# Kernel optimization log

Measured on AMD Instinct MI355X. Metric: run time of the kernel, lower is better.

## Reference

```python
import jax, jax.numpy as jnp
import numpy as np

EPS = 1e-3  # batch_norm_epsilon


def _lstm_last(xs, W, U, b):
    """Keras-order LSTM (gates i,f,g,o); returns last hidden state [B,H]."""
    B = xs.shape[0]
    H = U.shape[0]

    def step(carry, xt):
        h, c = carry
        z = xt @ W + h @ U + b  # [B, 4H]
        i, f, g, o = jnp.split(z, 4, axis=-1)
        i = jax.nn.sigmoid(i)
        f = jax.nn.sigmoid(f)
        g = jnp.tanh(g)
        o = jax.nn.sigmoid(o)
        c = f * c + i * g
        h = o * jnp.tanh(c)
        return (h, c), None

    init = (jnp.zeros((B, H), xs.dtype), jnp.zeros((B, H), xs.dtype))
    (h, _), _ = jax.lax.scan(step, init, jnp.swapaxes(xs, 0, 1))
    return h


def setup_inputs() -> dict:
    key = jax.random.key(0)
    ks = jax.random.split(key, 10)
    B, T, C, H = 32, 512, 512, 512
    s_in = 1.0 / np.sqrt(C)
    s_rec = 1.0 / np.sqrt(H)
    return {
        "x": jax.random.normal(ks[0], (B, T, C), jnp.float32),
        # BatchNorm params (inference / moving stats)
        "gamma": jnp.ones((C,), jnp.float32),
        "beta": jnp.zeros((C,), jnp.float32),
        "moving_mean": jax.random.normal(ks[1], (C,), jnp.float32) * 0.1,
        "moving_var": jnp.abs(jax.random.normal(ks[2], (C,), jnp.float32)) * 0.1 + 1.0,
        # forward-direction LSTM
        "Wf": jax.random.normal(ks[3], (C, 4 * H), jnp.float32) * s_in,
        "Uf": jax.random.normal(ks[4], (H, 4 * H), jnp.float32) * s_rec,
        "bf": jnp.zeros((4 * H,), jnp.float32),
        # backward-direction LSTM
        "Wb": jax.random.normal(ks[5], (C, 4 * H), jnp.float32) * s_in,
        "Ub": jax.random.normal(ks[6], (H, 4 * H), jnp.float32) * s_rec,
        "bb": jnp.zeros((4 * H,), jnp.float32),
    }


def reference(x, gamma, beta, moving_mean, moving_var, Wf, Uf, bf, Wb, Ub, bb):
    # BatchNorm (inference) over last axis
    inv = jax.lax.rsqrt(moving_var + EPS)
    xn = (x - moving_mean) * inv * gamma + beta
    # Bidirectional LSTM, merge_mode='concat', return_sequences=False
    h_fwd = _lstm_last(xn, Wf, Uf, bf)
    h_bwd = _lstm_last(xn[:, ::-1, :], Wb, Ub, bb)
    return jnp.concatenate([h_fwd, h_bwd], axis=-1)  # [B, 2H]
```

## Files before the change

### kernel.cpp

```cpp
#include <hip/hip_runtime.h>
#include <stdint.h>

typedef __attribute__((ext_vector_type(8))) short short8;
typedef __attribute__((ext_vector_type(4))) float f32x4;
typedef __attribute__((ext_vector_type(2))) float f32x2;

#define NB 32
#define NT 512
#define NC 512
#define NH 512
#define NG 2048
#define WPD 32
#define NWG 64
#define UPW 16

__device__ __forceinline__ float bf2f(unsigned short u){
  union { unsigned int i; float f; } v; v.i = ((unsigned int)u) << 16; return v.f;
}
__device__ __forceinline__ unsigned short f2bf(float f){
  union { float f; unsigned int i; } v; v.f = f;
  unsigned int r = v.i + 0x7fffu + ((v.i >> 16) & 1u);
  return (unsigned short)(r >> 16);
}
__device__ __forceinline__ bool dt_fp32(const void* gamma){
  return ((const unsigned short*)gamma)[0] != 0x3F80;
}
__device__ __forceinline__ float ldv(const void* p, size_t i, bool f32){
  return f32 ? ((const float*)p)[i] : bf2f(((const unsigned short*)p)[i]);
}
__device__ __forceinline__ short8 frag_from_f32(const float* p){
  short8 r;
  #pragma unroll
  for (int j = 0; j < 8; ++j) r[j] = (short)f2bf(p[j]);
  return r;
}
__device__ __forceinline__ float sigm(float x){ return 1.f/(1.f + __expf(-x)); }
__device__ __forceinline__ float tanh_(float x){ return 1.f - 2.f/(1.f + __expf(2.f*x)); }

__device__ __forceinline__ unsigned int llc_load_u32(const unsigned int* p){
  unsigned int r;
  asm volatile("global_load_dword %0, %1, off sc0 sc1\n\ts_waitcnt vmcnt(0)"
               : "=v"(r) : "v"(p) : "memory");
  return r;
}
__device__ __forceinline__ void llc_store_u32(unsigned int* p, unsigned int v){
  asm volatile("global_store_dword %0, %1, off sc0 sc1" :: "v"(p), "v"(v) : "memory");
}
__device__ __forceinline__ void llc_load_hfrags(const unsigned short* p0,
                                                const unsigned short* p1,
                                                short8 hf[4][2]){
  asm volatile(
    "global_load_dwordx4 %0, %8, off sc0 sc1\n\t"
    "global_load_dwordx4 %1, %8, off offset:64 sc0 sc1\n\t"
    "global_load_dwordx4 %2, %8, off offset:128 sc0 sc1\n\t"
    "global_load_dwordx4 %3, %8, off offset:192 sc0 sc1\n\t"
    "global_load_dwordx4 %4, %9, off sc0 sc1\n\t"
    "global_load_dwordx4 %5, %9, off offset:64 sc0 sc1\n\t"
    "global_load_dwordx4 %6, %9, off offset:128 sc0 sc1\n\t"
    "global_load_dwordx4 %7, %9, off offset:192 sc0 sc1\n\t"
    "s_waitcnt vmcnt(0)"
    : "=&v"(hf[0][0]), "=&v"(hf[1][0]), "=&v"(hf[2][0]), "=&v"(hf[3][0]),
      "=&v"(hf[0][1]), "=&v"(hf[1][1]), "=&v"(hf[2][1]), "=&v"(hf[3][1])
    : "v"(p0), "v"(p1) : "memory");
}

__global__ void k_init(const void* __restrict__ gamma,
                       const void* __restrict__ beta,
                       const void* __restrict__ mmean,
                       const void* __restrict__ mvar,
                       float* __restrict__ scale, float* __restrict__ shift,
                       unsigned short* __restrict__ hbuf, unsigned int* __restrict__ flags){
  bool f32 = dt_fp32(gamma);
  int tid = blockIdx.x * 256 + threadIdx.x;
  if (blockIdx.x == 0){
    for (int c = threadIdx.x; c < NC; c += 256){
      float s = ldv(gamma, c, f32) * rsqrtf(ldv(mvar, c, f32) + 1e-3f);
      scale[c] = s;
      shift[c] = ldv(beta, c, f32) - ldv(mmean, c, f32) * s;
    }
    if (threadIdx.x < 64) flags[threadIdx.x] = 0u;
  }
  for (int i = tid; i < 2*2*NB*NH; i += gridDim.x * 256) hbuf[i] = 0;
}

__global__ void k_xcast(const void* __restrict__ x, const void* __restrict__ gamma,
                        unsigned short* __restrict__ x2){
  bool f32 = dt_fp32(gamma);
  int i = blockIdx.x * 256 + threadIdx.x;
  int c8 = i & 63;
  int rest = i >> 6;
  int t = rest & (NT - 1);
  int b = rest >> 9;
  size_t src = ((size_t)b * NT + t) * NC + c8 * 8;
  size_t dst = ((size_t)t * NB + b) * NC + c8 * 8;
  unsigned int pk[4];
  if (f32){
    const float* p = (const float*)x + src;
    #pragma unroll
    for (int j = 0; j < 4; ++j)
      pk[j] = (unsigned int)f2bf(p[2*j]) | ((unsigned int)f2bf(p[2*j+1]) << 16);
  } else {
    __builtin_memcpy(pk, (const unsigned short*)x + src, 16);
  }
  __builtin_memcpy(x2 + dst, pk, 16);
}

__global__ void k_bias(const void* __restrict__ Wf, const void* __restrict__ Wb,
                       const void* __restrict__ bfv, const void* __restrict__ bbv,
                       const void* __restrict__ gamma,
                       const float* __restrict__ shift, float* __restrict__ bias){
  bool f32 = dt_fp32(gamma);
  int id = blockIdx.x * 256 + threadIdx.x;
  int dir = id >> 11, n = id & 2047;
  const void* W = dir ? Wb : Wf;
  const void* b = dir ? bbv : bfv;
  float acc = ldv(b, n, f32);
  for (int c = 0; c < NC; ++c) acc += shift[c] * ldv(W, (size_t)c * NG + n, f32);
  bias[id] = acc;
}

__global__ __launch_bounds__(256, 1) void k_lstm(
    const void* __restrict__ x, const unsigned short* __restrict__ x2, int use_x2,
    const void* __restrict__ Wf, const void* __restrict__ Uf,
    const void* __restrict__ Wb, const void* __restrict__ Ub,
    const void* __restrict__ gamma,
    const float* __restrict__ scale, const float* __restrict__ bias,
    unsigned short* __restrict__ hbuf, unsigned int* __restrict__ flags,
    void* __restrict__ out){
  __shared__ float zbuf[4][NB][68];

  bool f32 = dt_fp32(gamma);
  int wg   = blockIdx.x;
  int dir  = wg & 1;
  int wgd  = wg >> 1;
  int ubase = wgd * UPW;
  const void* W = dir ? Wb : Wf;
  const void* U = dir ? Ub : Uf;
  int tid  = threadIdx.x;
  int lane = tid & 63, wave = tid >> 6;
  int m = lane & 15, q = lane >> 4;

  short8 bw[4][4], bu[4][4];
  #pragma unroll
  for (int kcl = 0; kcl < 4; ++kcl){
    int kc = wave * 4 + kcl;
    #pragma unroll
    for (int g = 0; g < 4; ++g){
      int col = g * NH + ubase + m;
      short8 vw, vu;
      #pragma unroll
      for (int j = 0; j < 8; ++j){
        int k = kc * 32 + q * 8 + j;
        vu[j] = (short)f2bf(ldv(U, (size_t)k * NG + col, f32));
        vw[j] = (short)f2bf(scale[k] * ldv(W, (size_t)k * NG + col, f32));
      }
      bw[kcl][g] = vw; bu[kcl][g] = vu;
    }
  }

  int pb = tid >> 3, pu2 = (tid & 7) * 2;
  float bias_r[2][4];
  #pragma unroll
  for (int g = 0; g < 4; ++g){
    bias_r[0][g] = bias[dir * NG + g * NH + ubase + pu2];
    bias_r[1][g] = bias[dir * NG + g * NH + ubase + pu2 + 1];
  }
  float cst[2] = {0.f, 0.f};

  unsigned int* myflags = flags + dir * 32;
  unsigned int* ownflag = myflags + wgd;
  unsigned short* hb0 = hbuf + (size_t)dir * 2 * NB * NH;

  short8 xf[4][2];
  {
    int tt0 = dir ? (NT - 1) : 0;
    #pragma unroll
    for (int kcl = 0; kcl < 4; ++kcl){
      int kc = wave * 4 + kcl;
      #pragma unroll
      for (int mt = 0; mt < 2; ++mt){
        if (use_x2){
          size_t xi = ((size_t)tt0 * NB + (mt * 16 + m)) * NC + kc * 32 + q * 8;
          __builtin_memcpy(&xf[kcl][mt], x2 + xi, 16);
        } else {
          size_t xi = ((size_t)(mt * 16 + m) * NT + tt0) * NC + kc * 32 + q * 8;
          if (f32) xf[kcl][mt] = frag_from_f32((const float*)x + xi);
          else     __builtin_memcpy(&xf[kcl][mt], (const unsigned short*)x + xi, 16);
        }
      }
    }
  }

  #pragma unroll 1
  for (int t = 0; t < NT; ++t){
    const unsigned short* hcur = hb0 + (size_t)(t & 1) * NB * NH;
    unsigned short* hnext = hb0 + (size_t)((t + 1) & 1) * NB * NH;

    f32x4 acc[4][2];
    #pragma unroll
    for (int g = 0; g < 4; ++g){
      acc[g][0] = (f32x4){0.f,0.f,0.f,0.f};
      acc[g][1] = (f32x4){0.f,0.f,0.f,0.f};
    }

    #pragma unroll
    for (int kcl = 0; kcl < 4; ++kcl)
      #pragma unroll
      for (int mt = 0; mt < 2; ++mt)
        #pragma unroll
        for (int g = 0; g < 4; ++g)
          acc[g][mt] = __builtin_amdgcn_mfma_f32_16x16x32_bf16(xf[kcl][mt], bw[kcl][g], acc[g][mt], 0, 0, 0);

    if (t < NT - 1){
      int ttn = dir ? (NT - 2 - t) : (t + 1);
      #pragma unroll
      for (int kcl = 0; kcl < 4; ++kcl){
        int kc = wave * 4 + kcl;
        #pragma unroll
        for (int mt = 0; mt < 2; ++mt){
          if (use_x2){
            size_t xi = ((size_t)ttn * NB + (mt * 16 + m)) * NC + kc * 32 + q * 8;
            __builtin_memcpy(&xf[kcl][mt], x2 + xi, 16);
          } else {
            size_t xi = ((size_t)(mt * 16 + m) * NT + ttn) * NC + kc * 32 + q * 8;
            if (f32) xf[kcl][mt] = frag_from_f32((const float*)x + xi);
            else     __builtin_memcpy(&xf[kcl][mt], (const unsigned short*)x + xi, 16);
          }
        }
      }
    }

    if (t > 0){
      unsigned int tgt = (unsigned int)t;
      while (true){
        unsigned int v = llc_load_u32(myflags + (lane & 31));
        if (__all((int)(v >= tgt))) break;
      }
    }

    short8 hf[4][2];
    llc_load_hfrags(hcur + (size_t)m * NH + wave * 128 + q * 8,
                    hcur + (size_t)(16 + m) * NH + wave * 128 + q * 8, hf);
    #pragma unroll
    for (int kcl = 0; kcl < 4; ++kcl)
      #pragma unroll
      for (int mt = 0; mt < 2; ++mt)
        #pragma unroll
        for (int g = 0; g < 4; ++g)
          acc[g][mt] = __builtin_amdgcn_mfma_f32_16x16x32_bf16(hf[kcl][mt], bu[kcl][g], acc[g][mt], 0, 0, 0);

    #pragma unroll
    for (int g = 0; g < 4; ++g)
      #pragma unroll
      for (int mt = 0; mt < 2; ++mt)
        #pragma unroll
        for (int r = 0; r < 4; ++r)
          zbuf[wave][mt * 16 + q * 4 + r][g * 16 + m] = acc[g][mt][r];
    __syncthreads();

    float z[2][4];
    #pragma unroll
    for (int g = 0; g < 4; ++g){ z[0][g] = bias_r[0][g]; z[1][g] = bias_r[1][g]; }
    #pragma unroll
    for (int w = 0; w < 4; ++w)
      #pragma unroll
      for (int g = 0; g < 4; ++g){
        f32x2 v = *(const f32x2*)&zbuf[w][pb][g * 16 + pu2];
        z[0][g] += v[0]; z[1][g] += v[1];
      }
    float hv[2];
    #pragma unroll
    for (int j = 0; j < 2; ++j){
      float iv = sigm(z[j][0]), fv = sigm(z[j][1]), gv = tanh_(z[j][2]), ov = sigm(z[j][3]);
      cst[j] = fv * cst[j] + iv * gv;
      hv[j] = ov * tanh_(cst[j]);
    }

    if (t == NT - 1){
      size_t o0 = (size_t)pb * (2 * NH) + dir * NH + ubase + pu2;
      if (f32){
        f32x2 ov2 = {hv[0], hv[1]};
        *(f32x2*)&((float*)out)[o0] = ov2;
      } else {
        unsigned int pk = (unsigned int)f2bf(hv[0]) | ((unsigned int)f2bf(hv[1]) << 16);
        *(unsigned int*)&((unsigned short*)out)[o0] = pk;
      }
      break;
    }

    {
      unsigned int pk = (unsigned int)f2bf(hv[0]) | ((unsigned int)f2bf(hv[1]) << 16);
      llc_store_u32((unsigned int*)(hnext + (size_t)pb * NH + ubase + pu2), pk);
    }

    __syncthreads();
    if (tid == 0) llc_store_u32(ownflag, (unsigned int)(t + 1));
  }
}

extern "C" void kernel_launch(void* const* d_in, const int* in_sizes, int n_in,
                              void* d_out, int out_size, void* d_ws, size_t ws_size,
                              hipStream_t stream){
  const void* x     = d_in[0];
  const void* gamma = d_in[1];
  const void* beta  = d_in[2];
  const void* mmean = d_in[3];
  const void* mvar  = d_in[4];
  const void* Wf    = d_in[5];
  const void* Uf    = d_in[6];
  const void* bfv   = d_in[7];
  const void* Wb    = d_in[8];
  const void* Ub    = d_in[9];
  const void* bbv   = d_in[10];

  char* ws = (char*)d_ws;
  float* scale = (float*)(ws + 0);
  float* shift = (float*)(ws + 2048);
  float* bias  = (float*)(ws + 4096);
  unsigned short* hbuf = (unsigned short*)(ws + 20480);
  unsigned int* flags  = (unsigned int*)(ws + 20480 + 131072);
  size_t x2_off = 20480 + 131072 + 4096;
  unsigned short* x2 = (unsigned short*)(ws + x2_off);
  size_t x2_bytes = (size_t)NT * NB * NC * 2;
  int use_x2 = (ws_size >= x2_off + x2_bytes) ? 1 : 0;

  hipLaunchKernelGGL(k_init, dim3(64),  dim3(256), 0, stream,
                     gamma, beta, mmean, mvar, scale, shift, hbuf, flags);
  if (use_x2)
    hipLaunchKernelGGL(k_xcast, dim3((NB*NT*NC/8)/256), dim3(256), 0, stream,
                       x, gamma, x2);
  hipLaunchKernelGGL(k_bias, dim3(16),  dim3(256), 0, stream,
                     Wf, Wb, bfv, bbv, gamma, shift, bias);
  hipLaunchKernelGGL(k_lstm, dim3(NWG), dim3(256), 0, stream,
                     x, x2, use_x2, Wf, Uf, Wb, Ub, gamma, scale, bias, hbuf, flags, d_out);
}
```

Before: 2.052 ms.

## Replace per-step flag barrier with step-tagged hidden-state words polled directly

Each hidden value is now stored as a 32-bit word holding bf16 data in the high half and the timestep tag in the low half. Consumers poll the hidden-state fragments themselves until every tag matches, instead of spinning on per-workgroup flags and then loading h. This removes the separate flag store, the extra __syncthreads before it, and a dependent load round trip. The hidden loads are also issued before the input-projection MFMAs so they overlap that work, and zbuf is double-buffered by step parity so the trailing barrier can go. The cost is twice the hidden-buffer traffic, more registers for the raw words, and repeated reissue of 16 loads while the tags are not yet current.

```diff
diff --git a/kernel.cpp b/kernel.cpp
--- a/kernel.cpp
+++ b/kernel.cpp
@@ -4,6 +4,8 @@
 typedef __attribute__((ext_vector_type(8))) short short8;
 typedef __attribute__((ext_vector_type(4))) float f32x4;
 typedef __attribute__((ext_vector_type(2))) float f32x2;
+typedef __attribute__((ext_vector_type(4))) unsigned int u32x4;
+typedef __attribute__((ext_vector_type(2))) unsigned int u32x2;
 
 #define NB 32
 #define NT 512
@@ -37,31 +39,46 @@
 __device__ __forceinline__ float sigm(float x){ return 1.f/(1.f + __expf(-x)); }
 __device__ __forceinline__ float tanh_(float x){ return 1.f - 2.f/(1.f + __expf(2.f*x)); }
 
-__device__ __forceinline__ unsigned int llc_load_u32(const unsigned int* p){
-  unsigned int r;
-  asm volatile("global_load_dword %0, %1, off sc0 sc1\n\ts_waitcnt vmcnt(0)"
-               : "=v"(r) : "v"(p) : "memory");
-  return r;
-}
-__device__ __forceinline__ void llc_store_u32(unsigned int* p, unsigned int v){
-  asm volatile("global_store_dword %0, %1, off sc0 sc1" :: "v"(p), "v"(v) : "memory");
-}
-__device__ __forceinline__ void llc_load_hfrags(const unsigned short* p0,
-                                                const unsigned short* p1,
-                                                short8 hf[4][2]){
+__device__ __forceinline__ unsigned int permhi(unsigned int hi, unsigned int lo){
+  return __builtin_amdgcn_perm(hi, lo, 0x07060302u);
+}
+
+__device__ __forceinline__ void poll_issue(const unsigned int* p0, const unsigned int* p1,
+                                           u32x4 r[16]){
   asm volatile(
-    "global_load_dwordx4 %0, %8, off sc0 sc1\n\t"
-    "global_load_dwordx4 %1, %8, off offset:64 sc0 sc1\n\t"
-    "global_load_dwordx4 %2, %8, off offset:128 sc0 sc1\n\t"
-    "global_load_dwordx4 %3, %8, off offset:192 sc0 sc1\n\t"
-    "global_load_dwordx4 %4, %9, off sc0 sc1\n\t"
-    "global_load_dwordx4 %5, %9, off offset:64 sc0 sc1\n\t"
-    "global_load_dwordx4 %6, %9, off offset:128 sc0 sc1\n\t"
-    "global_load_dwordx4 %7, %9, off offset:192 sc0 sc1\n\t"
-    "s_waitcnt vmcnt(0)"
-    : "=&v"(hf[0][0]), "=&v"(hf[1][0]), "=&v"(hf[2][0]), "=&v"(hf[3][0]),
-      "=&v"(hf[0][1]), "=&v"(hf[1][1]), "=&v"(hf[2][1]), "=&v"(hf[3][1])
+    "global_load_dwordx4 %0, %16, off sc0 sc1\n\t"
+    "global_load_dwordx4 %1, %16, off offset:16 sc0 sc1\n\t"
+    "global_load_dwordx4 %2, %16, off offset:128 sc0 sc1\n\t"
+    "global_load_dwordx4 %3, %16, off offset:144 sc0 sc1\n\t"
+    "global_load_dwordx4 %4, %16, off offset:256 sc0 sc1\n\t"
+    "global_load_dwordx4 %5, %16, off offset:272 sc0 sc1\n\t"
+    "global_load_dwordx4 %6, %16, off offset:384 sc0 sc1\n\t"
+    "global_load_dwordx4 %7, %16, off offset:400 sc0 sc1\n\t"
+    "global_load_dwordx4 %8, %17, off sc0 sc1\n\t"
+    "global_load_dwordx4 %9, %17, off offset:16 sc0 sc1\n\t"
+    "global_load_dwordx4 %10, %17, off offset:128 sc0 sc1\n\t"
+    "global_load_dwordx4 %11, %17, off offset:144 sc0 sc1\n\t"
+    "global_load_dwordx4 %12, %17, off offset:256 sc0 sc1\n\t"
+    "global_load_dwordx4 %13, %17, off offset:272 sc0 sc1\n\t"
+    "global_load_dwordx4 %14, %17, off offset:384 sc0 sc1\n\t"
+    "global_load_dwordx4 %15, %17, off offset:400 sc0 sc1"
+    : "=&v"(r[0]), "=&v"(r[1]), "=&v"(r[2]), "=&v"(r[3]),
+      "=&v"(r[4]), "=&v"(r[5]), "=&v"(r[6]), "=&v"(r[7]),
+      "=&v"(r[8]), "=&v"(r[9]), "=&v"(r[10]), "=&v"(r[11]),
+      "=&v"(r[12]), "=&v"(r[13]), "=&v"(r[14]), "=&v"(r[15])
     : "v"(p0), "v"(p1) : "memory");
+}
+__device__ __forceinline__ void poll_wait(u32x4 r[16]){
+  asm volatile("s_waitcnt vmcnt(0)"
+    : "+v"(r[0]), "+v"(r[1]), "+v"(r[2]), "+v"(r[3]),
+      "+v"(r[4]), "+v"(r[5]), "+v"(r[6]), "+v"(r[7]),
+      "+v"(r[8]), "+v"(r[9]), "+v"(r[10]), "+v"(r[11]),
+      "+v"(r[12]), "+v"(r[13]), "+v"(r[14]), "+v"(r[15])
+    :: "memory");
+}
+__device__ __forceinline__ void llc_store_b64(unsigned int* p, unsigned int lo, unsigned int hi){
+  u32x2 v; v[0] = lo; v[1] = hi;
+  asm volatile("global_store_dwordx2 %0, %1, off sc0 sc1" :: "v"(p), "v"(v) : "memory");
 }
 
 __global__ void k_init(const void* __restrict__ gamma,
@@ -69,7 +86,7 @@
                        const void* __restrict__ mmean,
                        const void* __restrict__ mvar,
                        float* __restrict__ scale, float* __restrict__ shift,
-                       unsigned short* __restrict__ hbuf, unsigned int* __restrict__ flags){
+                       unsigned int* __restrict__ hbuf){
   bool f32 = dt_fp32(gamma);
   int tid = blockIdx.x * 256 + threadIdx.x;
   if (blockIdx.x == 0){
@@ -78,9 +95,8 @@
       scale[c] = s;
       shift[c] = ldv(beta, c, f32) - ldv(mmean, c, f32) * s;
     }
-    if (threadIdx.x < 64) flags[threadIdx.x] = 0u;
-  }
-  for (int i = tid; i < 2*2*NB*NH; i += gridDim.x * 256) hbuf[i] = 0;
+  }
+  for (int i = tid; i < 2*2*NB*NH; i += gridDim.x * 256) hbuf[i] = 0u;
 }
 
 __global__ void k_xcast(const void* __restrict__ x, const void* __restrict__ gamma,
@@ -125,9 +141,8 @@
     const void* __restrict__ Wb, const void* __restrict__ Ub,
     const void* __restrict__ gamma,
     const float* __restrict__ scale, const float* __restrict__ bias,
-    unsigned short* __restrict__ hbuf, unsigned int* __restrict__ flags,
-    void* __restrict__ out){
-  __shared__ float zbuf[4][NB][68];
+    unsigned int* __restrict__ hbuf, void* __restrict__ out){
+  __shared__ float zbuf[2][4][NB][68];
 
   bool f32 = dt_fp32(gamma);
   int wg   = blockIdx.x;
@@ -167,9 +182,7 @@
   }
   float cst[2] = {0.f, 0.f};
 
-  unsigned int* myflags = flags + dir * 32;
-  unsigned int* ownflag = myflags + wgd;
-  unsigned short* hb0 = hbuf + (size_t)dir * 2 * NB * NH;
+  unsigned int* hb32 = hbuf + (size_t)dir * 2 * NB * NH;
 
   short8 xf[4][2];
   {
@@ -193,8 +206,13 @@
 
   #pragma unroll 1
   for (int t = 0; t < NT; ++t){
-    const unsigned short* hcur = hb0 + (size_t)(t & 1) * NB * NH;
-    unsigned short* hnext = hb0 + (size_t)((t + 1) & 1) * NB * NH;
+    const unsigned int* hcur = hb32 + (size_t)(t & 1) * NB * NH;
+    unsigned int* hnext = hb32 + (size_t)((t + 1) & 1) * NB * NH;
+
+    u32x4 raw[16];
+    const unsigned int* p0 = hcur + (size_t)m * NH + wave * 128 + q * 8;
+    const unsigned int* p1 = p0 + (size_t)16 * NH;
+    poll_issue(p0, p1, raw);
 
     f32x4 acc[4][2];
     #pragma unroll
@@ -229,33 +247,46 @@
         }
       }
     }
-
-    if (t > 0){
-      unsigned int tgt = (unsigned int)t;
+    __builtin_amdgcn_sched_barrier(0);
+
+    {
+      unsigned int tg = (unsigned int)t;
       while (true){
-        unsigned int v = llc_load_u32(myflags + (lane & 31));
-        if (__all((int)(v >= tgt))) break;
-      }
-    }
-
-    short8 hf[4][2];
-    llc_load_hfrags(hcur + (size_t)m * NH + wave * 128 + q * 8,
-                    hcur + (size_t)(16 + m) * NH + wave * 128 + q * 8, hf);
-    #pragma unroll
-    for (int kcl = 0; kcl < 4; ++kcl)
+        poll_wait(raw);
+        unsigned int d = 0;
+        #pragma unroll
+        for (int i = 0; i < 16; ++i)
+          d |= (raw[i][0] ^ tg) | (raw[i][1] ^ tg) | (raw[i][2] ^ tg) | (raw[i][3] ^ tg);
+        if (__all((int)((d & 0xffffu) == 0u))) break;
+        poll_issue(p0, p1, raw);
+      }
+    }
+
+    #pragma unroll
+    for (int kcl = 0; kcl < 4; ++kcl){
+      #pragma unroll
+      for (int mt = 0; mt < 2; ++mt){
+        union { short8 s; unsigned int w[4]; } u;
+        u32x4 a = raw[mt * 8 + kcl * 2];
+        u32x4 b = raw[mt * 8 + kcl * 2 + 1];
+        u.w[0] = permhi(a[1], a[0]);
+        u.w[1] = permhi(a[3], a[2]);
+        u.w[2] = permhi(b[1], b[0]);
+        u.w[3] = permhi(b[3], b[2]);
+        #pragma unroll
+        for (int g = 0; g < 4; ++g)
+          acc[g][mt] = __builtin_amdgcn_mfma_f32_16x16x32_bf16(u.s, bu[kcl][g], acc[g][mt], 0, 0, 0);
+      }
+    }
+
+    int par = t & 1;
+    #pragma unroll
+    for (int g = 0; g < 4; ++g)
       #pragma unroll
       for (int mt = 0; mt < 2; ++mt)
         #pragma unroll
-        for (int g = 0; g < 4; ++g)
-          acc[g][mt] = __builtin_amdgcn_mfma_f32_16x16x32_bf16(hf[kcl][mt], bu[kcl][g], acc[g][mt], 0, 0, 0);
-
-    #pragma unroll
-    for (int g = 0; g < 4; ++g)
-      #pragma unroll
-      for (int mt = 0; mt < 2; ++mt)
-        #pragma unroll
         for (int r = 0; r < 4; ++r)
-          zbuf[wave][mt * 16 + q * 4 + r][g * 16 + m] = acc[g][mt][r];
+          zbuf[par][wave][mt * 16 + q * 4 + r][g * 16 + m] = acc[g][mt][r];
     __syncthreads();
 
     float z[2][4];
@@ -265,7 +296,7 @@
     for (int w = 0; w < 4; ++w)
       #pragma unroll
       for (int g = 0; g < 4; ++g){
-        f32x2 v = *(const f32x2*)&zbuf[w][pb][g * 16 + pu2];
+        f32x2 v = *(const f32x2*)&zbuf[par][w][pb][g * 16 + pu2];
         z[0][g] += v[0]; z[1][g] += v[1];
       }
     float hv[2];
@@ -289,12 +320,11 @@
     }
 
     {
-      unsigned int pk = (unsigned int)f2bf(hv[0]) | ((unsigned int)f2bf(hv[1]) << 16);
-      llc_store_u32((unsigned int*)(hnext + (size_t)pb * NH + ubase + pu2), pk);
-    }
-
-    __syncthreads();
-    if (tid == 0) llc_store_u32(ownflag, (unsigned int)(t + 1));
+      unsigned int tag1 = (unsigned int)(t + 1);
+      unsigned int w0 = ((unsigned int)f2bf(hv[0]) << 16) | tag1;
+      unsigned int w1 = ((unsigned int)f2bf(hv[1]) << 16) | tag1;
+      llc_store_b64(hnext + (size_t)pb * NH + ubase + pu2, w0, w1);
+    }
   }
 }
 
@@ -317,20 +347,19 @@
   float* scale = (float*)(ws + 0);
   float* shift = (float*)(ws + 2048);
   float* bias  = (float*)(ws + 4096);
-  unsigned short* hbuf = (unsigned short*)(ws + 20480);
-  unsigned int* flags  = (unsigned int*)(ws + 20480 + 131072);
-  size_t x2_off = 20480 + 131072 + 4096;
+  unsigned int* hbuf = (unsigned int*)(ws + 20480);
+  size_t x2_off = 20480 + 262144;
   unsigned short* x2 = (unsigned short*)(ws + x2_off);
   size_t x2_bytes = (size_t)NT * NB * NC * 2;
   int use_x2 = (ws_size >= x2_off + x2_bytes) ? 1 : 0;
 
   hipLaunchKernelGGL(k_init, dim3(64),  dim3(256), 0, stream,
-                     gamma, beta, mmean, mvar, scale, shift, hbuf, flags);
+                     gamma, beta, mmean, mvar, scale, shift, hbuf);
   if (use_x2)
     hipLaunchKernelGGL(k_xcast, dim3((NB*NT*NC/8)/256), dim3(256), 0, stream,
                        x, gamma, x2);
   hipLaunchKernelGGL(k_bias, dim3(16),  dim3(256), 0, stream,
                      Wf, Wb, bfv, bbv, gamma, shift, bias);
   hipLaunchKernelGGL(k_lstm, dim3(NWG), dim3(256), 0, stream,
-                     x, x2, use_x2, Wf, Uf, Wb, Ub, gamma, scale, bias, hbuf, flags, d_out);
-}
+                     x, x2, use_x2, Wf, Uf, Wb, Ub, gamma, scale, bias, hbuf, d_out);
+}
```

After: 2.812 ms. 37.0% more time.

## Fuse bias into LSTM kernel and switch to per-wave flags with pipelined polling

Applied to the files above, without the earlier changes.

Drops the separate bias-reduction kernel. The shift·W bias term is now accumulated during the weight-fragment load in the LSTM kernel and reduced with shuffles and shared memory. The block-wide barrier before the step flag is replaced by per-wave flags: each wave publishes its own completion and polls only the flags of the waves whose h slice it consumes. Flag polling keeps two loads in flight, and zbuf is double-buffered by step parity so the trailing barrier can go. This targets per-step synchronisation latency in the serial recurrence, at the cost of more flag traffic and subtler memory-ordering reasoning.

```diff
diff --git a/kernel.cpp b/kernel.cpp
--- a/kernel.cpp
+++ b/kernel.cpp
@@ -37,12 +37,6 @@
 __device__ __forceinline__ float sigm(float x){ return 1.f/(1.f + __expf(-x)); }
 __device__ __forceinline__ float tanh_(float x){ return 1.f - 2.f/(1.f + __expf(2.f*x)); }
 
-__device__ __forceinline__ unsigned int llc_load_u32(const unsigned int* p){
-  unsigned int r;
-  asm volatile("global_load_dword %0, %1, off sc0 sc1\n\ts_waitcnt vmcnt(0)"
-               : "=v"(r) : "v"(p) : "memory");
-  return r;
-}
 __device__ __forceinline__ void llc_store_u32(unsigned int* p, unsigned int v){
   asm volatile("global_store_dword %0, %1, off sc0 sc1" :: "v"(p), "v"(v) : "memory");
 }
@@ -78,7 +72,7 @@
       scale[c] = s;
       shift[c] = ldv(beta, c, f32) - ldv(mmean, c, f32) * s;
     }
-    if (threadIdx.x < 64) flags[threadIdx.x] = 0u;
+    flags[threadIdx.x] = 0u;
   }
   for (int i = tid; i < 2*2*NB*NH; i += gridDim.x * 256) hbuf[i] = 0;
 }
@@ -105,29 +99,16 @@
   __builtin_memcpy(x2 + dst, pk, 16);
 }
 
-__global__ void k_bias(const void* __restrict__ Wf, const void* __restrict__ Wb,
-                       const void* __restrict__ bfv, const void* __restrict__ bbv,
-                       const void* __restrict__ gamma,
-                       const float* __restrict__ shift, float* __restrict__ bias){
-  bool f32 = dt_fp32(gamma);
-  int id = blockIdx.x * 256 + threadIdx.x;
-  int dir = id >> 11, n = id & 2047;
-  const void* W = dir ? Wb : Wf;
-  const void* b = dir ? bbv : bfv;
-  float acc = ldv(b, n, f32);
-  for (int c = 0; c < NC; ++c) acc += shift[c] * ldv(W, (size_t)c * NG + n, f32);
-  bias[id] = acc;
-}
-
 __global__ __launch_bounds__(256, 1) void k_lstm(
     const void* __restrict__ x, const unsigned short* __restrict__ x2, int use_x2,
     const void* __restrict__ Wf, const void* __restrict__ Uf,
     const void* __restrict__ Wb, const void* __restrict__ Ub,
+    const void* __restrict__ bfv, const void* __restrict__ bbv,
     const void* __restrict__ gamma,
-    const float* __restrict__ scale, const float* __restrict__ bias,
+    const float* __restrict__ scale, const float* __restrict__ shift,
     unsigned short* __restrict__ hbuf, unsigned int* __restrict__ flags,
     void* __restrict__ out){
-  __shared__ float zbuf[4][NB][68];
+  __shared__ float zbuf[2][4][NB][68];
 
   bool f32 = dt_fp32(gamma);
   int wg   = blockIdx.x;
@@ -136,11 +117,13 @@
   int ubase = wgd * UPW;
   const void* W = dir ? Wb : Wf;
   const void* U = dir ? Ub : Uf;
+  const void* bvec = dir ? bbv : bfv;
   int tid  = threadIdx.x;
   int lane = tid & 63, wave = tid >> 6;
   int m = lane & 15, q = lane >> 4;
 
   short8 bw[4][4], bu[4][4];
+  float bp[4] = {0.f, 0.f, 0.f, 0.f};
   #pragma unroll
   for (int kcl = 0; kcl < 4; ++kcl){
     int kc = wave * 4 + kcl;
@@ -151,24 +134,44 @@
       #pragma unroll
       for (int j = 0; j < 8; ++j){
         int k = kc * 32 + q * 8 + j;
+        float wraw = ldv(W, (size_t)k * NG + col, f32);
         vu[j] = (short)f2bf(ldv(U, (size_t)k * NG + col, f32));
-        vw[j] = (short)f2bf(scale[k] * ldv(W, (size_t)k * NG + col, f32));
+        vw[j] = (short)f2bf(scale[k] * wraw);
+        bp[g] += shift[k] * wraw;
       }
       bw[kcl][g] = vw; bu[kcl][g] = vu;
     }
   }
+
+  #pragma unroll
+  for (int g = 0; g < 4; ++g){
+    bp[g] += __shfl_xor(bp[g], 16);
+    bp[g] += __shfl_xor(bp[g], 32);
+  }
+  float* bred = &zbuf[0][0][0][0];
+  if (q == 0){
+    #pragma unroll
+    for (int g = 0; g < 4; ++g) bred[wave * 64 + g * 16 + m] = bp[g];
+  }
+  __syncthreads();
 
   int pb = tid >> 3, pu2 = (tid & 7) * 2;
   float bias_r[2][4];
   #pragma unroll
-  for (int g = 0; g < 4; ++g){
-    bias_r[0][g] = bias[dir * NG + g * NH + ubase + pu2];
-    bias_r[1][g] = bias[dir * NG + g * NH + ubase + pu2 + 1];
-  }
+  for (int j = 0; j < 2; ++j)
+    #pragma unroll
+    for (int g = 0; g < 4; ++g){
+      float acc = ldv(bvec, g * NH + ubase + pu2 + j, f32);
+      #pragma unroll
+      for (int w = 0; w < 4; ++w) acc += bred[w * 64 + g * 16 + pu2 + j];
+      bias_r[j][g] = acc;
+    }
+  __syncthreads();
   float cst[2] = {0.f, 0.f};
 
-  unsigned int* myflags = flags + dir * 32;
-  unsigned int* ownflag = myflags + wgd;
+  unsigned int* myflags = flags + dir * 128;
+  unsigned int* ownflag = myflags + wgd * 4 + wave;
+  const unsigned int* fp = myflags + wave * 32 + (lane & 31);
   unsigned short* hb0 = hbuf + (size_t)dir * 2 * NB * NH;
 
   short8 xf[4][2];
@@ -190,6 +193,8 @@
       }
     }
   }
+
+  unsigned int fl0 = 0xffffffffu, fl1 = 0xffffffffu;
 
   #pragma unroll 1
   for (int t = 0; t < NT; ++t){
@@ -229,18 +234,26 @@
         }
       }
     }
+    __builtin_amdgcn_sched_barrier(0);
 
     if (t > 0){
       unsigned int tgt = (unsigned int)t;
+      asm volatile("global_load_dword %0, %1, off sc0 sc1" : "=v"(fl0) : "v"(fp) : "memory");
+      asm volatile("global_load_dword %0, %1, off sc0 sc1" : "=v"(fl1) : "v"(fp) : "memory");
       while (true){
-        unsigned int v = llc_load_u32(myflags + (lane & 31));
-        if (__all((int)(v >= tgt))) break;
+        asm volatile("s_waitcnt vmcnt(1)" : "+v"(fl0) :: "memory");
+        if (__all((int)(fl0 >= tgt))) break;
+        asm volatile("global_load_dword %0, %1, off sc0 sc1" : "=v"(fl0) : "v"(fp) : "memory");
+        asm volatile("s_waitcnt vmcnt(1)" : "+v"(fl1) :: "memory");
+        if (__all((int)(fl1 >= tgt))) break;
+        asm volatile("global_load_dword %0, %1, off sc0 sc1" : "=v"(fl1) : "v"(fp) : "memory");
       }
     }
 
     short8 hf[4][2];
     llc_load_hfrags(hcur + (size_t)m * NH + wave * 128 + q * 8,
                     hcur + (size_t)(16 + m) * NH + wave * 128 + q * 8, hf);
+    asm volatile("" : "+v"(fl0), "+v"(fl1));
     #pragma unroll
     for (int kcl = 0; kcl < 4; ++kcl)
       #pragma unroll
@@ -249,13 +262,14 @@
         for (int g = 0; g < 4; ++g)
           acc[g][mt] = __builtin_amdgcn_mfma_f32_16x16x32_bf16(hf[kcl][mt], bu[kcl][g], acc[g][mt], 0, 0, 0);
 
+    int par = t & 1;
     #pragma unroll
     for (int g = 0; g < 4; ++g)
       #pragma unroll
       for (int mt = 0; mt < 2; ++mt)
         #pragma unroll
         for (int r = 0; r < 4; ++r)
-          zbuf[wave][mt * 16 + q * 4 + r][g * 16 + m] = acc[g][mt][r];
+          zbuf[par][wave][mt * 16 + q * 4 + r][g * 16 + m] = acc[g][mt][r];
     __syncthreads();
 
     float z[2][4];
@@ -265,7 +279,7 @@
     for (int w = 0; w < 4; ++w)
       #pragma unroll
       for (int g = 0; g < 4; ++g){
-        f32x2 v = *(const f32x2*)&zbuf[w][pb][g * 16 + pu2];
+        f32x2 v = *(const f32x2*)&zbuf[par][w][pb][g * 16 + pu2];
         z[0][g] += v[0]; z[1][g] += v[1];
       }
     float hv[2];
@@ -291,10 +305,9 @@
     {
       unsigned int pk = (unsigned int)f2bf(hv[0]) | ((unsigned int)f2bf(hv[1]) << 16);
       llc_store_u32((unsigned int*)(hnext + (size_t)pb * NH + ubase + pu2), pk);
-    }
-
-    __syncthreads();
-    if (tid == 0) llc_store_u32(ownflag, (unsigned int)(t + 1));
+      asm volatile("s_waitcnt vmcnt(0)" ::: "memory");
+      if ((tid & 63) == 0) llc_store_u32(ownflag, (unsigned int)(t + 1));
+    }
   }
 }
 
@@ -316,7 +329,6 @@
   char* ws = (char*)d_ws;
   float* scale = (float*)(ws + 0);
   float* shift = (float*)(ws + 2048);
-  float* bias  = (float*)(ws + 4096);
   unsigned short* hbuf = (unsigned short*)(ws + 20480);
   unsigned int* flags  = (unsigned int*)(ws + 20480 + 131072);
   size_t x2_off = 20480 + 131072 + 4096;
@@ -329,8 +341,7 @@
   if (use_x2)
     hipLaunchKernelGGL(k_xcast, dim3((NB*NT*NC/8)/256), dim3(256), 0, stream,
                        x, gamma, x2);
-  hipLaunchKernelGGL(k_bias, dim3(16),  dim3(256), 0, stream,
-                     Wf, Wb, bfv, bbv, gamma, shift, bias);
   hipLaunchKernelGGL(k_lstm, dim3(NWG), dim3(256), 0, stream,
-                     x, x2, use_x2, Wf, Uf, Wb, Ub, gamma, scale, bias, hbuf, flags, d_out);
-}
+                     x, x2, use_x2, Wf, Uf, Wb, Ub, bfv, bbv, gamma, scale, shift,
+                     hbuf, flags, d_out);
+}
```

Result: slower. 2.142 ms (+4.4%).

## Split LSTM batch into halves per sync group and fuse bias into main kernel

Applied to the files above, without the earlier changes.

The work split changes from 32 workgroups per direction, each owning 16 hidden units for all 32 batch rows, to four independent groups (direction × batch half) of 16 workgroups, each owning 32 units for 16 batch rows. Each group syncs only among 16 peers on its own flags and h buffer, so fewer workgroups poll per step and each loads half as much h. The separate bias kernel is dropped and the folded BN-shift bias is computed inside each workgroup at startup. The trade-off is more U/W fragment registers per thread (8 N-tiles instead of 4), which adds register pressure, plus some extra startup work.

```diff
diff --git a/kernel.cpp b/kernel.cpp
--- a/kernel.cpp
+++ b/kernel.cpp
@@ -6,13 +6,14 @@
 typedef __attribute__((ext_vector_type(2))) float f32x2;
 
 #define NB 32
+#define NBH 16
 #define NT 512
 #define NC 512
 #define NH 512
 #define NG 2048
-#define WPD 32
+#define WPG 16
 #define NWG 64
-#define UPW 16
+#define UPW 32
 
 __device__ __forceinline__ float bf2f(unsigned short u){
   union { unsigned int i; float f; } v; v.i = ((unsigned int)u) << 16; return v.f;
@@ -46,22 +47,15 @@
 __device__ __forceinline__ void llc_store_u32(unsigned int* p, unsigned int v){
   asm volatile("global_store_dword %0, %1, off sc0 sc1" :: "v"(p), "v"(v) : "memory");
 }
-__device__ __forceinline__ void llc_load_hfrags(const unsigned short* p0,
-                                                const unsigned short* p1,
-                                                short8 hf[4][2]){
+__device__ __forceinline__ void llc_load_hfrags4(const unsigned short* p0, short8 hf[4]){
   asm volatile(
-    "global_load_dwordx4 %0, %8, off sc0 sc1\n\t"
-    "global_load_dwordx4 %1, %8, off offset:64 sc0 sc1\n\t"
-    "global_load_dwordx4 %2, %8, off offset:128 sc0 sc1\n\t"
-    "global_load_dwordx4 %3, %8, off offset:192 sc0 sc1\n\t"
-    "global_load_dwordx4 %4, %9, off sc0 sc1\n\t"
-    "global_load_dwordx4 %5, %9, off offset:64 sc0 sc1\n\t"
-    "global_load_dwordx4 %6, %9, off offset:128 sc0 sc1\n\t"
-    "global_load_dwordx4 %7, %9, off offset:192 sc0 sc1\n\t"
+    "global_load_dwordx4 %0, %4, off sc0 sc1\n\t"
+    "global_load_dwordx4 %1, %4, off offset:64 sc0 sc1\n\t"
+    "global_load_dwordx4 %2, %4, off offset:128 sc0 sc1\n\t"
+    "global_load_dwordx4 %3, %4, off offset:192 sc0 sc1\n\t"
     "s_waitcnt vmcnt(0)"
-    : "=&v"(hf[0][0]), "=&v"(hf[1][0]), "=&v"(hf[2][0]), "=&v"(hf[3][0]),
-      "=&v"(hf[0][1]), "=&v"(hf[1][1]), "=&v"(hf[2][1]), "=&v"(hf[3][1])
-    : "v"(p0), "v"(p1) : "memory");
+    : "=&v"(hf[0]), "=&v"(hf[1]), "=&v"(hf[2]), "=&v"(hf[3])
+    : "v"(p0) : "memory");
 }
 
 __global__ void k_init(const void* __restrict__ gamma,
@@ -78,9 +72,9 @@
       scale[c] = s;
       shift[c] = ldv(beta, c, f32) - ldv(mmean, c, f32) * s;
     }
-    if (threadIdx.x < 64) flags[threadIdx.x] = 0u;
-  }
-  for (int i = tid; i < 2*2*NB*NH; i += gridDim.x * 256) hbuf[i] = 0;
+    if (threadIdx.x < 128) flags[threadIdx.x] = 0u;
+  }
+  for (int i = tid; i < 4*2*NBH*NH; i += gridDim.x * 256) hbuf[i] = 0;
 }
 
 __global__ void k_xcast(const void* __restrict__ x, const void* __restrict__ gamma,
@@ -105,48 +99,40 @@
   __builtin_memcpy(x2 + dst, pk, 16);
 }
 
-__global__ void k_bias(const void* __restrict__ Wf, const void* __restrict__ Wb,
-                       const void* __restrict__ bfv, const void* __restrict__ bbv,
-                       const void* __restrict__ gamma,
-                       const float* __restrict__ shift, float* __restrict__ bias){
-  bool f32 = dt_fp32(gamma);
-  int id = blockIdx.x * 256 + threadIdx.x;
-  int dir = id >> 11, n = id & 2047;
-  const void* W = dir ? Wb : Wf;
-  const void* b = dir ? bbv : bfv;
-  float acc = ldv(b, n, f32);
-  for (int c = 0; c < NC; ++c) acc += shift[c] * ldv(W, (size_t)c * NG + n, f32);
-  bias[id] = acc;
-}
-
 __global__ __launch_bounds__(256, 1) void k_lstm(
     const void* __restrict__ x, const unsigned short* __restrict__ x2, int use_x2,
     const void* __restrict__ Wf, const void* __restrict__ Uf,
     const void* __restrict__ Wb, const void* __restrict__ Ub,
+    const void* __restrict__ bfv, const void* __restrict__ bbv,
     const void* __restrict__ gamma,
-    const float* __restrict__ scale, const float* __restrict__ bias,
+    const float* __restrict__ scale, const float* __restrict__ shift,
     unsigned short* __restrict__ hbuf, unsigned int* __restrict__ flags,
     void* __restrict__ out){
-  __shared__ float zbuf[4][NB][68];
+  __shared__ float zbuf[4][NBH][132];
+  __shared__ float fscr[256];
+  __shared__ float fb[128];
 
   bool f32 = dt_fp32(gamma);
   int wg   = blockIdx.x;
   int dir  = wg & 1;
-  int wgd  = wg >> 1;
+  int half = (wg >> 1) & 1;
+  int wgd  = wg >> 2;
+  int gidx = wg & 3;
   int ubase = wgd * UPW;
   const void* W = dir ? Wb : Wf;
   const void* U = dir ? Ub : Uf;
+  const void* bvec = dir ? bbv : bfv;
   int tid  = threadIdx.x;
   int lane = tid & 63, wave = tid >> 6;
   int m = lane & 15, q = lane >> 4;
 
-  short8 bw[4][4], bu[4][4];
+  short8 bw[4][8], bu[4][8];
   #pragma unroll
   for (int kcl = 0; kcl < 4; ++kcl){
     int kc = wave * 4 + kcl;
     #pragma unroll
-    for (int g = 0; g < 4; ++g){
-      int col = g * NH + ubase + m;
+    for (int nt = 0; nt < 8; ++nt){
+      int col = (nt >> 1) * NH + ubase + (nt & 1) * 16 + m;
       short8 vw, vu;
       #pragma unroll
       for (int j = 0; j < 8; ++j){
@@ -154,78 +140,82 @@
         vu[j] = (short)f2bf(ldv(U, (size_t)k * NG + col, f32));
         vw[j] = (short)f2bf(scale[k] * ldv(W, (size_t)k * NG + col, f32));
       }
-      bw[kcl][g] = vw; bu[kcl][g] = vu;
-    }
-  }
-
-  int pb = tid >> 3, pu2 = (tid & 7) * 2;
+      bw[kcl][nt] = vw; bu[kcl][nt] = vu;
+    }
+  }
+
+  {
+    int cidx = tid >> 1, kh = tid & 1;
+    int col = (cidx >> 5) * NH + ubase + (cidx & 31);
+    float a = 0.f;
+    for (int k = kh * 256; k < kh * 256 + 256; ++k)
+      a += shift[k] * ldv(W, (size_t)k * NG + col, f32);
+    fscr[tid] = a;
+    __syncthreads();
+    if (tid < 128)
+      fb[tid] = fscr[2*tid] + fscr[2*tid+1]
+              + ldv(bvec, (tid >> 5) * NH + ubase + (tid & 31), f32);
+    __syncthreads();
+  }
+
+  int pb = tid >> 4, pu2 = (tid & 15) * 2;
   float bias_r[2][4];
   #pragma unroll
-  for (int g = 0; g < 4; ++g){
-    bias_r[0][g] = bias[dir * NG + g * NH + ubase + pu2];
-    bias_r[1][g] = bias[dir * NG + g * NH + ubase + pu2 + 1];
-  }
+  for (int j = 0; j < 2; ++j)
+    #pragma unroll
+    for (int g = 0; g < 4; ++g) bias_r[j][g] = fb[g * 32 + pu2 + j];
   float cst[2] = {0.f, 0.f};
 
-  unsigned int* myflags = flags + dir * 32;
-  unsigned int* ownflag = myflags + wgd;
-  unsigned short* hb0 = hbuf + (size_t)dir * 2 * NB * NH;
-
-  short8 xf[4][2];
+  unsigned int* gflags  = flags + gidx * 32;
+  unsigned int* ownflag = gflags + wgd;
+  unsigned short* hb0 = hbuf + (size_t)gidx * 2 * NBH * NH;
+
+  short8 xf[4];
   {
     int tt0 = dir ? (NT - 1) : 0;
+    int b = half * 16 + m;
     #pragma unroll
     for (int kcl = 0; kcl < 4; ++kcl){
       int kc = wave * 4 + kcl;
-      #pragma unroll
-      for (int mt = 0; mt < 2; ++mt){
-        if (use_x2){
-          size_t xi = ((size_t)tt0 * NB + (mt * 16 + m)) * NC + kc * 32 + q * 8;
-          __builtin_memcpy(&xf[kcl][mt], x2 + xi, 16);
-        } else {
-          size_t xi = ((size_t)(mt * 16 + m) * NT + tt0) * NC + kc * 32 + q * 8;
-          if (f32) xf[kcl][mt] = frag_from_f32((const float*)x + xi);
-          else     __builtin_memcpy(&xf[kcl][mt], (const unsigned short*)x + xi, 16);
-        }
+      if (use_x2){
+        size_t xi = ((size_t)tt0 * NB + b) * NC + kc * 32 + q * 8;
+        __builtin_memcpy(&xf[kcl], x2 + xi, 16);
+      } else {
+        size_t xi = ((size_t)b * NT + tt0) * NC + kc * 32 + q * 8;
+        if (f32) xf[kcl] = frag_from_f32((const float*)x + xi);
+        else     __builtin_memcpy(&xf[kcl], (const unsigned short*)x + xi, 16);
       }
     }
   }
 
   #pragma unroll 1
   for (int t = 0; t < NT; ++t){
-    const unsigned short* hcur = hb0 + (size_t)(t & 1) * NB * NH;
-    unsigned short* hnext = hb0 + (size_t)((t + 1) & 1) * NB * NH;
-
-    f32x4 acc[4][2];
-    #pragma unroll
-    for (int g = 0; g < 4; ++g){
-      acc[g][0] = (f32x4){0.f,0.f,0.f,0.f};
-      acc[g][1] = (f32x4){0.f,0.f,0.f,0.f};
-    }
+    const unsigned short* hcur = hb0 + (size_t)(t & 1) * NBH * NH;
+    unsigned short* hnext = hb0 + (size_t)((t + 1) & 1) * NBH * NH;
+
+    f32x4 acc[8];
+    #pragma unroll
+    for (int nt = 0; nt < 8; ++nt) acc[nt] = (f32x4){0.f,0.f,0.f,0.f};
 
     #pragma unroll
     for (int kcl = 0; kcl < 4; ++kcl)
       #pragma unroll
-      for (int mt = 0; mt < 2; ++mt)
-        #pragma unroll
-        for (int g = 0; g < 4; ++g)
-          acc[g][mt] = __builtin_amdgcn_mfma_f32_16x16x32_bf16(xf[kcl][mt], bw[kcl][g], acc[g][mt], 0, 0, 0);
+      for (int nt = 0; nt < 8; ++nt)
+        acc[nt] = __builtin_amdgcn_mfma_f32_16x16x32_bf16(xf[kcl], bw[kcl][nt], acc[nt], 0, 0, 0);
 
     if (t < NT - 1){
       int ttn = dir ? (NT - 2 - t) : (t + 1);
+      int b = half * 16 + m;
       #pragma unroll
       for (int kcl = 0; kcl < 4; ++kcl){
         int kc = wave * 4 + kcl;
-        #pragma unroll
-        for (int mt = 0; mt < 2; ++mt){
-          if (use_x2){
-            size_t xi = ((size_t)ttn * NB + (mt * 16 + m)) * NC + kc * 32 + q * 8;
-            __builtin_memcpy(&xf[kcl][mt], x2 + xi, 16);
-          } else {
-            size_t xi = ((size_t)(mt * 16 + m) * NT + ttn) * NC + kc * 32 + q * 8;
-            if (f32) xf[kcl][mt] = frag_from_f32((const float*)x + xi);
-            else     __builtin_memcpy(&xf[kcl][mt], (const unsigned short*)x + xi, 16);
-          }
+        if (use_x2){
+          size_t xi = ((size_t)ttn * NB + b) * NC + kc * 32 + q * 8;
+          __builtin_memcpy(&xf[kcl], x2 + xi, 16);
+        } else {
+          size_t xi = ((size_t)b * NT + ttn) * NC + kc * 32 + q * 8;
+          if (f32) xf[kcl] = frag_from_f32((const float*)x + xi);
+          else     __builtin_memcpy(&xf[kcl], (const unsigned short*)x + xi, 16);
         }
       }
     }
@@ -233,29 +223,26 @@
     if (t > 0){
       unsigned int tgt = (unsigned int)t;
       while (true){
-        unsigned int v = llc_load_u32(myflags + (lane & 31));
+        unsigned int v = llc_load_u32(gflags + (lane & 15));
         if (__all((int)(v >= tgt))) break;
       }
     }
 
-    short8 hf[4][2];
-    llc_load_hfrags(hcur + (size_t)m * NH + wave * 128 + q * 8,
-                    hcur + (size_t)(16 + m) * NH + wave * 128 + q * 8, hf);
+    short8 hf[4];
+    llc_load_hfrags4(hcur + (size_t)m * NH + wave * 128 + q * 8, hf);
     #pragma unroll
     for (int kcl = 0; kcl < 4; ++kcl)
       #pragma unroll
-      for (int mt = 0; mt < 2; ++mt)
-        #pragma unroll
-        for (int g = 0; g < 4; ++g)
-          acc[g][mt] = __builtin_amdgcn_mfma_f32_16x16x32_bf16(hf[kcl][mt], bu[kcl][g], acc[g][mt], 0, 0, 0);
-
-    #pragma unroll
-    for (int g = 0; g < 4; ++g)
-      #pragma unroll
-      for (int mt = 0; mt < 2; ++mt)
-        #pragma unroll
-        for (int r = 0; r < 4; ++r)
-          zbuf[wave][mt * 16 + q * 4 + r][g * 16 + m] = acc[g][mt][r];
+      for (int nt = 0; nt < 8; ++nt)
+        acc[nt] = __builtin_amdgcn_mfma_f32_16x16x32_bf16(hf[kcl], bu[kcl][nt], acc[nt], 0, 0, 0);
+
+    #pragma unroll
+    for (int nt = 0; nt < 8; ++nt){
+      int cb = (nt >> 1) * 32 + (nt & 1) * 16 + m;
+      #pragma unroll
+      for (int r = 0; r < 4; ++r)
+        zbuf[wave][q * 4 + r][cb] = acc[nt][r];
+    }
     __syncthreads();
 
     float z[2][4];
@@ -265,7 +252,7 @@
     for (int w = 0; w < 4; ++w)
       #pragma unroll
       for (int g = 0; g < 4; ++g){
-        f32x2 v = *(const f32x2*)&zbuf[w][pb][g * 16 + pu2];
+        f32x2 v = *(const f32x2*)&zbuf[w][pb][g * 32 + pu2];
         z[0][g] += v[0]; z[1][g] += v[1];
       }
     float hv[2];
@@ -277,7 +264,7 @@
     }
 
     if (t == NT - 1){
-      size_t o0 = (size_t)pb * (2 * NH) + dir * NH + ubase + pu2;
+      size_t o0 = (size_t)(half * 16 + pb) * (2 * NH) + dir * NH + ubase + pu2;
       if (f32){
         f32x2 ov2 = {hv[0], hv[1]};
         *(f32x2*)&((float*)out)[o0] = ov2;
@@ -316,7 +303,6 @@
   char* ws = (char*)d_ws;
   float* scale = (float*)(ws + 0);
   float* shift = (float*)(ws + 2048);
-  float* bias  = (float*)(ws + 4096);
   unsigned short* hbuf = (unsigned short*)(ws + 20480);
   unsigned int* flags  = (unsigned int*)(ws + 20480 + 131072);
   size_t x2_off = 20480 + 131072 + 4096;
@@ -329,8 +315,7 @@
   if (use_x2)
     hipLaunchKernelGGL(k_xcast, dim3((NB*NT*NC/8)/256), dim3(256), 0, stream,
                        x, gamma, x2);
-  hipLaunchKernelGGL(k_bias, dim3(16),  dim3(256), 0, stream,
-                     Wf, Wb, bfv, bbv, gamma, shift, bias);
   hipLaunchKernelGGL(k_lstm, dim3(NWG), dim3(256), 0, stream,
-                     x, x2, use_x2, Wf, Uf, Wb, Ub, gamma, scale, bias, hbuf, flags, d_out);
-}
+                     x, x2, use_x2, Wf, Uf, Wb, Ub, bfv, bbv, gamma, scale, shift,
+                     hbuf, flags, d_out);
+}
```

After: 1.853 ms. -9.7%, faster.
